# Kernel optimization log

Hardware: AMD Instinct MI355X
Metric: run time of the kernel (lower is better)

## Reference

```python
import jax, jax.numpy as jnp
import numpy as np

EPS_MASK = 1e-9   # module fills masked scores with eps, NOT -inf
LN_EPS = 1e-5

def _layer_norm(x, g, b):
    mu = jnp.mean(x, axis=-1, keepdims=True)
    var = jnp.mean(jnp.square(x - mu), axis=-1, keepdims=True)
    return (x - mu) * jax.lax.rsqrt(var + LN_EPS) * g + b

def _mha(q_in, k_in, v_in, wq, bq, wk, bk, wv, bv, wo, bo, mask, nhead):
    B, Sq, D = q_in.shape
    dk = D // nhead
    def proj(x, w, b):
        y = x @ w + b                                   # [B,S,D]
        return y.reshape(B, -1, nhead, dk).transpose(0, 2, 1, 3)  # [B,h,S,dk]
    q, k, v = proj(q_in, wq, bq), proj(k_in, wk, bk), proj(v_in, wv, bv)
    scores = jnp.einsum('bhqd,bhkd->bhqk', q, k) / np.sqrt(dk).astype(q.dtype)
    if mask is not None:
        scores = jnp.where(mask[:, None, :, :] == 0, jnp.asarray(EPS_MASK, scores.dtype), scores)
    p = jax.nn.softmax(scores, axis=-1)                 # dropout = identity (eval)
    x = jnp.einsum('bhqk,bhkd->bhqd', p, v)
    x = x.transpose(0, 2, 1, 3).reshape(B, Sq, D)
    return x @ wo + bo

def _forward_post(tgt, memory, tgt_pos, memory_pos, tgt_mask, memory_mask, p):
    nhead = 8
    # self-attention (q=k=tgt+pos, v=tgt)
    q = tgt + tgt_pos
    sa = _mha(q, q, tgt, p['sa_wq'], p['sa_bq'], p['sa_wk'], p['sa_bk'],
              p['sa_wv'], p['sa_bv'], p['sa_wo'], p['sa_bo'], tgt_mask, nhead)
    tgt = _layer_norm(tgt + sa, p['ln1_g'], p['ln1_b'])
    # cross-attention (q=tgt+tgt_pos, k=memory+memory_pos, v=memory)
    mq = tgt + tgt_pos
    mk = memory + memory_pos
    ca = _mha(mq, mk, memory, p['ca_wq'], p['ca_bq'], p['ca_wk'], p['ca_bk'],
              p['ca_wv'], p['ca_bv'], p['ca_wo'], p['ca_bo'], memory_mask, nhead)
    tgt = _layer_norm(tgt + ca, p['ln2_g'], p['ln2_b'])
    # FFN
    h = jax.nn.relu(tgt @ p['mlp_w1'] + p['mlp_b1'])
    ff = h @ p['mlp_w2'] + p['mlp_b2']
    return _layer_norm(tgt + ff, p['ln3_g'], p['ln3_b'])

def setup_inputs() -> dict:
    key = jax.random.key(0)
    B, S, M, D, H = 4, 1024, 1024, 512, 2048
    ks = iter(jax.random.split(key, 40))
    d = {
        'tgt': jax.random.normal(next(ks), (B, S, D), jnp.float32),
        'memory': jax.random.normal(next(ks), (B, M, D), jnp.float32),
        'tgt_pos': jax.random.normal(next(ks), (B, S, D), jnp.float32),
        'memory_pos': jax.random.normal(next(ks), (B, M, D), jnp.float32),
        'tgt_mask': jax.random.randint(next(ks), (B, S, S), 0, 2, jnp.int32),
        'memory_mask': jax.random.randint(next(ks), (B, S, M), 0, 2, jnp.int32),
    }
    for pre in ('sa', 'ca'):
        for nm in ('q', 'k', 'v', 'o'):
            d[f'{pre}_w{nm}'] = jax.random.normal(next(ks), (D, D), jnp.float32) * 0.02
            d[f'{pre}_b{nm}'] = jnp.zeros((D,), jnp.float32)
    for i in (1, 2, 3):
        d[f'ln{i}_g'] = jnp.ones((D,), jnp.float32)
        d[f'ln{i}_b'] = jnp.zeros((D,), jnp.float32)
    d['mlp_w1'] = jax.random.normal(next(ks), (D, H), jnp.float32) * 0.02
    d['mlp_b1'] = jnp.zeros((H,), jnp.float32)
    d['mlp_w2'] = jax.random.normal(next(ks), (H, D), jnp.float32) * 0.02
    d['mlp_b2'] = jnp.zeros((D,), jnp.float32)
    return d

def reference(tgt, memory, tgt_pos, memory_pos, tgt_mask, memory_mask,
              sa_wq, sa_bq, sa_wk, sa_bk, sa_wv, sa_bv, sa_wo, sa_bo,
              ca_wq, ca_bq, ca_wk, ca_bk, ca_wv, ca_bv, ca_wo, ca_bo,
              ln1_g, ln1_b, ln2_g, ln2_b, ln3_g, ln3_b,
              mlp_w1, mlp_b1, mlp_w2, mlp_b2):
    p = dict(sa_wq=sa_wq, sa_bq=sa_bq, sa_wk=sa_wk, sa_bk=sa_bk, sa_wv=sa_wv,
             sa_bv=sa_bv, sa_wo=sa_wo, sa_bo=sa_bo, ca_wq=ca_wq, ca_bq=ca_bq,
             ca_wk=ca_wk, ca_bk=ca_bk, ca_wv=ca_wv, ca_bv=ca_bv, ca_wo=ca_wo,
             ca_bo=ca_bo, ln1_g=ln1_g, ln1_b=ln1_b, ln2_g=ln2_g, ln2_b=ln2_b,
             ln3_g=ln3_g, ln3_b=ln3_b, mlp_w1=mlp_w1, mlp_b1=mlp_b1,
             mlp_w2=mlp_w2, mlp_b2=mlp_b2)
    return _forward_post(tgt, memory, tgt_pos, memory_pos, tgt_mask, memory_mask, p)
```

## Files before the change

kernel.cpp:

```cpp
#include <hip/hip_runtime.h>
#include <stdint.h>

typedef unsigned int u32;
typedef unsigned long long u64;
typedef unsigned short u16;
typedef __attribute__((ext_vector_type(8))) __bf16 bf16x8;
typedef __attribute__((ext_vector_type(4))) float f32x4;

#define DEV __device__ __forceinline__

DEV u16 f2bf(float f) {
    u32 x = __builtin_bit_cast(u32, f);
    u32 r = (x + 0x7FFFu + ((x >> 16) & 1u)) >> 16;
    return (u16)r;
}

DEV float bf2f(u16 x) {
    u32 u = (u32)x << 16;
    return __builtin_bit_cast(float, u);
}

DEV void unp8(uint4 u, float* f) {
    f[0] = bf2f((u16)u.x); f[1] = bf2f((u16)(u.x >> 16));
    f[2] = bf2f((u16)u.y); f[3] = bf2f((u16)(u.y >> 16));
    f[4] = bf2f((u16)u.z); f[5] = bf2f((u16)(u.z >> 16));
    f[6] = bf2f((u16)u.w); f[7] = bf2f((u16)(u.w >> 16));
}

DEV bf16x8 ldg8(const u16* p) {
    return __builtin_bit_cast(bf16x8, *(const uint4*)p);
}

DEV u32 pk2(float a, float b) {
    return (u32)f2bf(a) | ((u32)f2bf(b) << 16);
}

DEV void g2l16(const u16* g, u16* l) {
    __builtin_amdgcn_global_load_lds(
        (const __attribute__((address_space(1))) u32*)g,
        (__attribute__((address_space(3))) u32*)l, 16, 0, 0);
}

DEV f32x4 mfma16(bf16x8 a, bf16x8 b, f32x4 c) {
    return __builtin_amdgcn_mfma_f32_16x16x32_bf16(a, b, c, 0, 0, 0);
}

struct ProArgs {
    const float* w[10];
    u16* wtbase;
    const float4 *tgt, *tpos, *mem, *mpos;
    ushort4 *qin, *tgtb, *memb, *mkb, *tposb;
    const int4 *m1, *m2;
    u32 *o1, *o2;
};
__global__ __launch_bounds__(256) void prologue_kernel(ProArgs a) {
    const int bx = blockIdx.x, t = threadIdx.x;
    if (bx < 10240) {
        int z = bx >> 10, bxx = bx & 1023;
        int Kd = (z == 9) ? 2048 : 512;
        int Nd = (z == 8) ? 2048 : 512;
        size_t off = (z < 8) ? (size_t)z * 262144
                             : (z == 8 ? (size_t)2097152 : (size_t)3145728);
        u16* out = a.wtbase + off;
        int nx = Nd / 32;
        int txile = bxx % nx, tyile = bxx / nx;
        if (tyile >= Kd / 32) return;
        const float* w = a.w[z];
        __shared__ float tl[32][33];
        int tx = t & 31, ty = t >> 5;
#pragma unroll
        for (int j = 0; j < 4; ++j)
            tl[ty + j * 8][tx] = w[(size_t)(tyile * 32 + ty + j * 8) * Nd + txile * 32 + tx];
        __syncthreads();
#pragma unroll
        for (int j = 0; j < 4; ++j)
            out[(size_t)(txile * 32 + ty + j * 8) * Kd + tyile * 32 + tx] = f2bf(tl[tx][ty + j * 8]);
    } else if (bx < 12288) {
        int i = (bx - 10240) * 256 + t;
        float4 tt = a.tgt[i], p = a.tpos[i], m = a.mem[i], mp = a.mpos[i];
        a.qin[i]  = make_ushort4(f2bf(tt.x + p.x), f2bf(tt.y + p.y), f2bf(tt.z + p.z), f2bf(tt.w + p.w));
        a.tgtb[i] = make_ushort4(f2bf(tt.x), f2bf(tt.y), f2bf(tt.z), f2bf(tt.w));
        a.memb[i] = make_ushort4(f2bf(m.x), f2bf(m.y), f2bf(m.z), f2bf(m.w));
        a.mkb[i]  = make_ushort4(f2bf(m.x + mp.x), f2bf(m.y + mp.y), f2bf(m.z + mp.z), f2bf(m.w + mp.w));
        a.tposb[i]= make_ushort4(f2bf(p.x), f2bf(p.y), f2bf(p.z), f2bf(p.w));
    } else {
        int i = (bx - 12288) * 256 + t;
        const int n8 = 524288;
        bool first = i < n8;
        int idx = first ? i : i - n8;
        const int4* src = first ? a.m1 : a.m2;
        int4 x = src[idx * 2], y = src[idx * 2 + 1];
        u32 by = (u32)(x.x != 0) | ((u32)(x.y != 0) << 1) | ((u32)(x.z != 0) << 2) |
                 ((u32)(x.w != 0) << 3) | ((u32)(y.x != 0) << 4) | ((u32)(y.y != 0) << 5) |
                 ((u32)(y.z != 0) << 6) | ((u32)(y.w != 0) << 7);
        u32 w = by | (__shfl_down(by, 1) << 8) | (__shfl_down(by, 2) << 16) |
                (__shfl_down(by, 3) << 24);
        if ((t & 3) == 0) (first ? a.o1 : a.o2)[idx >> 2] = w;
    }
}

struct GemmSet {
    const u16* A; const u16* W; const float* bias; void* out;
    float oscale; int epi; int k0; int klen;
};
struct GemmArgs5 { GemmSet s[5]; };

template <int BM, int BN>
__global__ __launch_bounds__(256) void gemm_kernel(GemmArgs5 args, int M, int N, int Kd) {
    constexpr int MF = BM / 32, NF = BN / 32;
    const GemmSet gs = args.s[blockIdx.z];
    const u16* __restrict__ A = gs.A;
    const u16* __restrict__ W = gs.W;
    const int t = threadIdx.x;
    const int lane = t & 63;
    const int g = lane >> 4, r16 = lane & 15;
    const int wave = t >> 6;
    const int wm = wave >> 1, wn = wave & 1;
    const int nwg = gridDim.x * gridDim.y;
    const int fid = blockIdx.y * gridDim.x + blockIdx.x;
    const int qq = nwg >> 3;
    const int lid = (fid & 7) * qq + (fid >> 3);
    const int m0 = (lid / gridDim.x) * BM, n0 = (lid % gridDim.x) * BN;

    __shared__ __align__(16) u16 As[BM * 64];
    __shared__ __align__(16) u16 Bs[BN * 64];

    f32x4 acc[MF][NF];
#pragma unroll
    for (int m = 0; m < MF; ++m)
#pragma unroll
        for (int n = 0; n < NF; ++n) acc[m][n] = f32x4{0.f, 0.f, 0.f, 0.f};

    const int kend = gs.k0 + gs.klen;
    for (int kk = gs.k0; kk < kend; kk += 64) {
        __syncthreads();
#pragma unroll
        for (int i = 0; i < BM / 32; ++i) {
            int cid = t + i * 256, row = cid >> 3, c = cid & 7;
            g2l16(A + (size_t)(m0 + row) * Kd + kk + ((c ^ (row & 7)) << 3), &As[cid << 3]);
        }
#pragma unroll
        for (int i = 0; i < BN / 32; ++i) {
            int cid = t + i * 256, row = cid >> 3, c = cid & 7;
            g2l16(W + (size_t)(n0 + row) * Kd + kk + ((c ^ (row & 7)) << 3), &Bs[cid << 3]);
        }
        __syncthreads();
#pragma unroll
        for (int ks = 0; ks < 2; ++ks) {
            bf16x8 af[MF], bfr[NF];
#pragma unroll
            for (int m = 0; m < MF; ++m) {
                int row = wm * (MF * 16) + m * 16 + r16;
                af[m] = *(const bf16x8*)&As[(row << 6) + (((ks * 4 + g) ^ (row & 7)) << 3)];
            }
#pragma unroll
            for (int n = 0; n < NF; ++n) {
                int row = wn * (NF * 16) + n * 16 + r16;
                bfr[n] = *(const bf16x8*)&Bs[(row << 6) + (((ks * 4 + g) ^ (row & 7)) << 3)];
            }
#pragma unroll
            for (int m = 0; m < MF; ++m)
#pragma unroll
                for (int n = 0; n < NF; ++n)
                    acc[m][n] = mfma16(af[m], bfr[n], acc[m][n]);
        }
    }
    const int epi = gs.epi;
#pragma unroll
    for (int m = 0; m < MF; ++m) {
        int row0 = m0 + wm * (MF * 16) + m * 16 + g * 4;
#pragma unroll
        for (int n = 0; n < NF; ++n) {
            int col = n0 + wn * (NF * 16) + n * 16 + r16;
            float bv = gs.bias ? gs.bias[col] : 0.f;
            float v[4];
#pragma unroll
            for (int r = 0; r < 4; ++r) v[r] = (acc[m][n][r] + bv) * gs.oscale;
            if (epi == 1) {
#pragma unroll
                for (int r = 0; r < 4; ++r) v[r] = fmaxf(v[r], 0.f);
            }
            if (epi == 3) {
                int bb = row0 >> 10, s = row0 & 1023;
                u16* o = (u16*)gs.out +
                         ((size_t)(bb * 8 + (col >> 6)) * 64 + (col & 63)) * 1024 + s;
                *(ushort4*)o = make_ushort4(f2bf(v[0]), f2bf(v[1]), f2bf(v[2]), f2bf(v[3]));
            } else {
                u16* o = (u16*)gs.out;
#pragma unroll
                for (int r = 0; r < 4; ++r) o[(size_t)(row0 + r) * N + col] = f2bf(v[r]);
            }
        }
    }
}

__global__ __launch_bounds__(512, 4) void attn_part_kernel(
    const u16* __restrict__ Q, const u16* __restrict__ K,
    const u16* __restrict__ VT, const u32* __restrict__ mb,
    u16* __restrict__ OP, float2* __restrict__ ML) {
    constexpr int Lq = 1024, Lk = 1024, NCH = 8;
    const int t = threadIdx.x, lane = t & 63, wave = t >> 6;
    const int g = lane >> 4, r16 = lane & 15;
    const int h = blockIdx.x;
    const int b = blockIdx.y >> 1, p = blockIdx.y & 1;
    const int bh = b * 8 + h;
    const int q0 = blockIdx.z * 128 + wave * 16;
    const int kc0 = p * (Lk >> 1);

    __shared__ __align__(16) u16 Ks[2][64][64];
    __shared__ __align__(16) u16 Vs[2][64][64];
    __shared__ __align__(16) u16 Pl[8][16][72];

    const size_t qrow = (size_t)b * Lq + q0 + r16;
    const u16* qp = Q + qrow * 512 + h * 64 + g * 8;
    bf16x8 qb0 = ldg8(qp), qb1 = ldg8(qp + 32);
    const u32* mrow = mb + qrow * (Lk >> 5);

    const int sid = t & 255;
    const bool isK = t < 256;
    const int s1 = sid, s2 = sid + 256;
    const int r1 = s1 >> 3, c1 = s1 & 7;
    const int r2 = s2 >> 3, c2 = s2 & 7;
    const u16 *sgA, *sgB;
    if (isK) {
        const u16* kbase = K + (size_t)b * Lk * 512 + h * 64;
        sgA = kbase + (size_t)(kc0 + r1) * 512 + ((c1 ^ (r1 & 7)) << 3);
        sgB = kbase + (size_t)(kc0 + r2) * 512 + ((c2 ^ (r2 & 7)) << 3);
    } else {
        const u16* vbase = VT + (size_t)bh * 64 * Lk + kc0;
        sgA = vbase + (size_t)r1 * Lk + ((c1 ^ (r1 & 7)) << 3);
        sgB = vbase + (size_t)r2 * Lk + ((c2 ^ (r2 & 7)) << 3);
    }
    const size_t adv = isK ? (size_t)64 * 512 : 64;
    u16* const base = isK ? &Ks[0][0][0] : &Vs[0][0][0];
    u16* const slA = base + s1 * 8;
    u16* const slB = base + s2 * 8;

    f32x4 acc[4];
#pragma unroll
    for (int dt = 0; dt < 4; ++dt) acc[dt] = f32x4{0.f, 0.f, 0.f, 0.f};
    float mrun = -INFINITY, lrun = 0.f;
    const f32x4 zf = {0.f, 0.f, 0.f, 0.f};

    g2l16(sgA, slA);
    g2l16(sgB, slB);
    __syncthreads();

#pragma unroll
    for (int c = 0; c < NCH; ++c) {
        const int buf = c & 1, nbuf = buf ^ 1;
        const int kc = kc0 + c * 64;
        if (c + 1 < NCH) {
            g2l16(sgA + (size_t)(c + 1) * adv, slA + nbuf * 4096);
            g2l16(sgB + (size_t)(c + 1) * adv, slB + nbuf * 4096);
        }
        const u16* kb = &Ks[buf][0][0];
        const u16* vb = &Vs[buf][0][0];
        f32x4 s[4];
#pragma unroll
        for (int j = 0; j < 4; ++j) {
            int row = j * 16 + r16;
            bf16x8 ka0 = *(const bf16x8*)(kb + row * 64 + ((g ^ (row & 7)) << 3));
            bf16x8 ka1 = *(const bf16x8*)(kb + row * 64 + (((4 + g) ^ (row & 7)) << 3));
            s[j] = mfma16(ka0, qb0, zf);
            s[j] = mfma16(ka1, qb1, s[j]);
        }
        u32 mw0 = mrow[kc >> 5], mw1 = mrow[(kc >> 5) + 1];
        float sv[16];
#pragma unroll
        for (int j = 0; j < 4; ++j) {
            u32 w = (j < 2) ? mw0 : mw1;
            int bbase = (16 * j) & 31;
#pragma unroll
            for (int r = 0; r < 4; ++r) {
                int bit = bbase + g * 4 + r;
                sv[4 * j + r] = ((w >> bit) & 1) ? s[j][r] : 1e-9f;
            }
        }
        float tm = fmaxf(fmaxf(fmaxf(sv[0], sv[1]), fmaxf(sv[2], sv[3])),
                         fmaxf(fmaxf(sv[4], sv[5]), fmaxf(sv[6], sv[7])));
        float tm2 = fmaxf(fmaxf(fmaxf(sv[8], sv[9]), fmaxf(sv[10], sv[11])),
                          fmaxf(fmaxf(sv[12], sv[13]), fmaxf(sv[14], sv[15])));
        tm = fmaxf(tm, tm2);
        tm = fmaxf(tm, __shfl_xor(tm, 16));
        tm = fmaxf(tm, __shfl_xor(tm, 32));
        if (!__all(tm <= mrun + 8.f)) {
            float mn = fmaxf(mrun, tm);
            float alpha = __expf(mrun - mn);
            mrun = mn;
            lrun *= alpha;
#pragma unroll
            for (int r = 0; r < 4; ++r) {
                float ar = __shfl(alpha, g * 4 + r);
#pragma unroll
                for (int dt = 0; dt < 4; ++dt) acc[dt][r] *= ar;
            }
        }
        float ts = 0.f;
#pragma unroll
        for (int j = 0; j < 16; ++j) { sv[j] = __expf(sv[j] - mrun); ts += sv[j]; }
        ts += __shfl_xor(ts, 16);
        ts += __shfl_xor(ts, 32);
        lrun += ts;

#pragma unroll
        for (int j = 0; j < 4; ++j) {
            uint2 u;
            u.x = pk2(sv[4 * j], sv[4 * j + 1]);
            u.y = pk2(sv[4 * j + 2], sv[4 * j + 3]);
            *(uint2*)&Pl[wave][r16][16 * j + g * 4] = u;
        }
        bf16x8 pf0 = *(const bf16x8*)&Pl[wave][r16][g * 8];
        bf16x8 pf1 = *(const bf16x8*)&Pl[wave][r16][32 + g * 8];
#pragma unroll
        for (int dt = 0; dt < 4; ++dt) {
            int row = dt * 16 + r16;
            bf16x8 vf0 = *(const bf16x8*)(vb + row * 64 + ((g ^ (row & 7)) << 3));
            bf16x8 vf1 = *(const bf16x8*)(vb + row * 64 + (((4 + g) ^ (row & 7)) << 3));
            acc[dt] = mfma16(pf0, vf0, acc[dt]);
            acc[dt] = mfma16(pf1, vf1, acc[dt]);
        }
        __syncthreads();
    }

    if (lane < 16)
        ML[(size_t)p * 32768 + (size_t)bh * 1024 + q0 + lane] = make_float2(mrun, lrun);
    const size_t obase = (size_t)p * 2097152 + ((size_t)bh * 1024 + q0) * 64;
#pragma unroll
    for (int dt = 0; dt < 4; ++dt)
#pragma unroll
        for (int r = 0; r < 4; ++r)
            OP[obase + (size_t)(g * 4 + r) * 64 + dt * 16 + r16] = f2bf(acc[dt][r]);
}

__global__ __launch_bounds__(256) void attn_combine_kernel(
    const u16* __restrict__ OP, const float2* __restrict__ ML, u16* __restrict__ O) {
    int gid = blockIdx.x * 256 + threadIdx.x;
    int row = gid >> 3, seg = gid & 7;
    size_t idx = (size_t)row * 64 + seg * 8;
    float2 ml0 = ML[row], ml1 = ML[32768 + row];
    float M = fmaxf(ml0.x, ml1.x);
    float w0 = __expf(ml0.x - M), w1 = __expf(ml1.x - M);
    float rden = 1.f / (ml0.y * w0 + ml1.y * w1);
    w0 *= rden; w1 *= rden;
    float a[8], b[8];
    unp8(*(const uint4*)(OP + idx), a);
    unp8(*(const uint4*)(OP + 2097152 + idx), b);
    int bh = row >> 10, q = row & 1023;
    int bb = bh >> 3, h = bh & 7;
    u16* o = O + ((size_t)(bb * 1024 + q)) * 512 + h * 64 + seg * 8;
    uint4 r;
    r.x = pk2(a[0] * w0 + b[0] * w1, a[1] * w0 + b[1] * w1);
    r.y = pk2(a[2] * w0 + b[2] * w1, a[3] * w0 + b[3] * w1);
    r.z = pk2(a[4] * w0 + b[4] * w1, a[5] * w0 + b[5] * w1);
    r.w = pk2(a[6] * w0 + b[6] * w1, a[7] * w0 + b[7] * w1);
    *(uint4*)o = r;
}

template <int MODE>
__global__ __launch_bounds__(256) void ln_kernel(
    const u16* __restrict__ a, const u16* __restrict__ b1, const u16* __restrict__ b2,
    const float* __restrict__ gam, const float* __restrict__ bet,
    const u16* __restrict__ pos,
    u16* __restrict__ yb, u16* __restrict__ qb, float* __restrict__ yf) {
    const int lane = threadIdx.x & 63;
    const int row = blockIdx.x * 4 + (threadIdx.x >> 6);
    const size_t base = (size_t)row * 512 + lane * 8;
    float av[8], bv[8], cv[8];
    unp8(*(const uint4*)(a + base), av);
    unp8(*(const uint4*)(b1 + base), bv);
    unp8(*(const uint4*)(b2 + base), cv);
    float x[8];
#pragma unroll
    for (int j = 0; j < 8; ++j) x[j] = av[j] + bv[j] + cv[j];
    float s1 = 0.f, s2 = 0.f;
#pragma unroll
    for (int j = 0; j < 8; ++j) { s1 += x[j]; s2 += x[j] * x[j]; }
#pragma unroll
    for (int d = 1; d < 64; d <<= 1) { s1 += __shfl_xor(s1, d); s2 += __shfl_xor(s2, d); }
    float mean = s1 * (1.f / 512.f);
    float var = s2 * (1.f / 512.f) - mean * mean;
    float rs = rsqrtf(var + 1e-5f);
    float4 gv0 = ((const float4*)(gam + lane * 8))[0];
    float4 gv1 = ((const float4*)(gam + lane * 8))[1];
    float4 be0 = ((const float4*)(bet + lane * 8))[0];
    float4 be1 = ((const float4*)(bet + lane * 8))[1];
    float gg[8] = {gv0.x, gv0.y, gv0.z, gv0.w, gv1.x, gv1.y, gv1.z, gv1.w};
    float bb[8] = {be0.x, be0.y, be0.z, be0.w, be1.x, be1.y, be1.z, be1.w};
    float y[8];
#pragma unroll
    for (int j = 0; j < 8; ++j) y[j] = (x[j] - mean) * rs * gg[j] + bb[j];
    if (MODE == 2) {
        ((float4*)(yf + base))[0] = make_float4(y[0], y[1], y[2], y[3]);
        ((float4*)(yf + base))[1] = make_float4(y[4], y[5], y[6], y[7]);
        return;
    }
    uint4 r;
    r.x = pk2(y[0], y[1]); r.y = pk2(y[2], y[3]);
    r.z = pk2(y[4], y[5]); r.w = pk2(y[6], y[7]);
    *(uint4*)(yb + base) = r;
    if (MODE == 0) {
        float pv[8];
        unp8(*(const uint4*)(pos + base), pv);
        uint4 q;
        q.x = pk2(y[0] + pv[0], y[1] + pv[1]);
        q.y = pk2(y[2] + pv[2], y[3] + pv[3]);
        q.z = pk2(y[4] + pv[4], y[5] + pv[5]);
        q.w = pk2(y[6] + pv[6], y[7] + pv[7]);
        *(uint4*)(qb + base) = q;
    }
}

extern "C" void kernel_launch(void* const* d_in, const int* in_sizes, int n_in,
                              void* d_out, int out_size, void* d_ws, size_t ws_size,
                              hipStream_t stream) {
    (void)in_sizes; (void)n_in; (void)out_size; (void)ws_size;
    const float* tgt      = (const float*)d_in[0];
    const float* memory   = (const float*)d_in[1];
    const float* tgt_pos  = (const float*)d_in[2];
    const float* mem_pos  = (const float*)d_in[3];
    const int*   tgt_mask = (const int*)d_in[4];
    const int*   mem_mask = (const int*)d_in[5];
    const float* sa_b[4] = {(const float*)d_in[7], (const float*)d_in[9],
                            (const float*)d_in[11], (const float*)d_in[13]};
    const float* ca_b[4] = {(const float*)d_in[15], (const float*)d_in[17],
                            (const float*)d_in[19], (const float*)d_in[21]};
    const float* ln1_g = (const float*)d_in[22]; const float* ln1_b = (const float*)d_in[23];
    const float* ln2_g = (const float*)d_in[24]; const float* ln2_b = (const float*)d_in[25];
    const float* ln3_g = (const float*)d_in[26]; const float* ln3_b = (const float*)d_in[27];
    const float* mlp_b1 = (const float*)d_in[29];
    const float* mlp_b2 = (const float*)d_in[31];

    const size_t MiB = 1024 * 1024;
    char* ws = (char*)d_ws;
    u16*  WT  = (u16*)(ws + 0);
    u32*  MBS = (u32*)(ws + 8 * MiB);
    u32*  MBC = (u32*)(ws + 8 * MiB + 512 * 1024);
    u16*  QIN = (u16*)(ws + 9 * MiB);
    u16*  TGTB= (u16*)(ws + 13 * MiB);
    u16*  MEMB= (u16*)(ws + 17 * MiB);
    u16*  MKB = (u16*)(ws + 21 * MiB);
    u16*  QM  = (u16*)(ws + 25 * MiB);
    u16*  KMS = (u16*)(ws + 29 * MiB);
    u16*  KMC = (u16*)(ws + 33 * MiB);
    u16*  VTS = (u16*)(ws + 37 * MiB);
    u16*  VTC = (u16*)(ws + 41 * MiB);
    u16*  ATNB= (u16*)(ws + 45 * MiB);
    u16*  P1B = (u16*)(ws + 49 * MiB);
    u16*  X1B = (u16*)(ws + 53 * MiB);
    u16*  MQB = (u16*)(ws + 57 * MiB);
    u16*  X2B = (u16*)(ws + 61 * MiB);
    u16*  TPB = (u16*)(ws + 65 * MiB);
    u16*  P2B = (u16*)(ws + 69 * MiB);
    u16*  FFH = (u16*)(ws + 9 * MiB);
    u16*  OPB = (u16*)(ws + 96 * MiB);
    float2* MLB = (float2*)(ws + 120 * MiB);

    u16* wt[10];
    for (int z = 0; z < 8; ++z) wt[z] = WT + (size_t)z * 262144;
    wt[8] = WT + 2097152;
    wt[9] = WT + 3145728;

    ProArgs pa;
    pa.w[0] = (const float*)d_in[6];  pa.w[1] = (const float*)d_in[8];
    pa.w[2] = (const float*)d_in[10]; pa.w[3] = (const float*)d_in[12];
    pa.w[4] = (const float*)d_in[14]; pa.w[5] = (const float*)d_in[16];
    pa.w[6] = (const float*)d_in[18]; pa.w[7] = (const float*)d_in[20];
    pa.w[8] = (const float*)d_in[28]; pa.w[9] = (const float*)d_in[30];
    pa.wtbase = WT;
    pa.tgt = (const float4*)tgt; pa.tpos = (const float4*)tgt_pos;
    pa.mem = (const float4*)memory; pa.mpos = (const float4*)mem_pos;
    pa.qin = (ushort4*)QIN; pa.tgtb = (ushort4*)TGTB;
    pa.memb = (ushort4*)MEMB; pa.mkb = (ushort4*)MKB;
    pa.tposb = (ushort4*)TPB;
    pa.m1 = (const int4*)tgt_mask; pa.m2 = (const int4*)mem_mask;
    pa.o1 = MBS; pa.o2 = MBC;
    prologue_kernel<<<16384, 256, 0, stream>>>(pa);

    GemmArgs5 ga;
    ga.s[0] = {QIN,  wt[0], sa_b[0], QM,  0.125f, 0, 0, 512};
    ga.s[1] = {QIN,  wt[1], sa_b[1], KMS, 1.f,    0, 0, 512};
    ga.s[2] = {TGTB, wt[2], sa_b[2], VTS, 1.f,    3, 0, 512};
    ga.s[3] = {MKB,  wt[5], ca_b[1], KMC, 1.f,    0, 0, 512};
    ga.s[4] = {MEMB, wt[6], ca_b[2], VTC, 1.f,    3, 0, 512};
    gemm_kernel<128, 64><<<dim3(8, 32, 5), 256, 0, stream>>>(ga, 4096, 512, 512);
    attn_part_kernel<<<dim3(8, 8, 8), 512, 0, stream>>>(QM, KMS, VTS, MBS, OPB, MLB);
    attn_combine_kernel<<<1024, 256, 0, stream>>>(OPB, MLB, ATNB);
    ga.s[0] = {ATNB, wt[3], sa_b[3], P1B, 1.f, 0, 0,   256};
    ga.s[1] = {ATNB, wt[3], nullptr, P2B, 1.f, 0, 256, 256};
    ga.s[2] = ga.s[0]; ga.s[3] = ga.s[0]; ga.s[4] = ga.s[0];
    gemm_kernel<64, 64><<<dim3(8, 64, 2), 256, 0, stream>>>(ga, 4096, 512, 512);
    ln_kernel<0><<<1024, 256, 0, stream>>>(TGTB, P1B, P2B, ln1_g, ln1_b, TPB, X1B, MQB, nullptr);

    ga.s[0] = {MQB, wt[4], ca_b[0], QM, 0.125f, 0, 0, 512};
    ga.s[1] = ga.s[0]; ga.s[2] = ga.s[0]; ga.s[3] = ga.s[0]; ga.s[4] = ga.s[0];
    gemm_kernel<64, 64><<<dim3(8, 64, 1), 256, 0, stream>>>(ga, 4096, 512, 512);
    attn_part_kernel<<<dim3(8, 8, 8), 512, 0, stream>>>(QM, KMC, VTC, MBC, OPB, MLB);
    attn_combine_kernel<<<1024, 256, 0, stream>>>(OPB, MLB, ATNB);
    ga.s[0] = {ATNB, wt[7], ca_b[3], P1B, 1.f, 0, 0,   256};
    ga.s[1] = {ATNB, wt[7], nullptr, P2B, 1.f, 0, 256, 256};
    ga.s[2] = ga.s[0]; ga.s[3] = ga.s[0]; ga.s[4] = ga.s[0];
    gemm_kernel<64, 64><<<dim3(8, 64, 2), 256, 0, stream>>>(ga, 4096, 512, 512);
    ln_kernel<1><<<1024, 256, 0, stream>>>(X1B, P1B, P2B, ln2_g, ln2_b, nullptr, X2B, nullptr, nullptr);

    ga.s[0] = {X2B, wt[8], mlp_b1, FFH, 1.f, 1, 0, 512};
    ga.s[1] = ga.s[0]; ga.s[2] = ga.s[0]; ga.s[3] = ga.s[0]; ga.s[4] = ga.s[0];
    gemm_kernel<128, 64><<<dim3(32, 32, 1), 256, 0, stream>>>(ga, 4096, 2048, 512);
    ga.s[0] = {FFH, wt[9], mlp_b2, P1B, 1.f, 0, 0,    1024};
    ga.s[1] = {FFH, wt[9], nullptr, P2B, 1.f, 0, 1024, 1024};
    ga.s[2] = ga.s[0]; ga.s[3] = ga.s[0]; ga.s[4] = ga.s[0];
    gemm_kernel<64, 64><<<dim3(8, 64, 2), 256, 0, stream>>>(ga, 4096, 512, 2048);
    ln_kernel<2><<<1024, 256, 0, stream>>>(X2B, P1B, P2B, ln3_g, ln3_b, nullptr,
                                           nullptr, nullptr, (float*)d_out);
}
```

Before: 158.8 us.

## Split attention keys four ways and fold log2e into Q scale for exp2

The flash-attention partial kernel now splits the 1024 keys into four chunks instead of two, doubling the block count. The combine kernel merges four partial outputs using their running max and sum. Separately, the Q projection scale now includes log2(e), so the softmax uses the native exp2 instruction. The mask fill value and the rescale threshold are scaled to match. The extra split adds partial-output traffic and combine work, and relies on the OP/ML scratch buffers being large enough for four partitions.

```diff
diff --git a/kernel.cpp b/kernel.cpp
--- a/kernel.cpp
+++ b/kernel.cpp
@@ -33,6 +33,10 @@
 
 DEV u32 pk2(float a, float b) {
     return (u32)f2bf(a) | ((u32)f2bf(b) << 16);
+}
+
+DEV float ex2(float x) {
+    return __builtin_amdgcn_exp2f(x);
 }
 
 DEV void g2l16(const u16* g, u16* l) {
@@ -198,14 +202,16 @@
     const u16* __restrict__ Q, const u16* __restrict__ K,
     const u16* __restrict__ VT, const u32* __restrict__ mb,
     u16* __restrict__ OP, float2* __restrict__ ML) {
-    constexpr int Lq = 1024, Lk = 1024, NCH = 8;
+    constexpr int Lq = 1024, Lk = 1024, NCH = 4;
+    constexpr float MFILL = 1.442695041e-9f;
+    constexpr float DTHR  = 11.5415603f;
     const int t = threadIdx.x, lane = t & 63, wave = t >> 6;
     const int g = lane >> 4, r16 = lane & 15;
     const int h = blockIdx.x;
-    const int b = blockIdx.y >> 1, p = blockIdx.y & 1;
+    const int b = blockIdx.y >> 2, p = blockIdx.y & 3;
     const int bh = b * 8 + h;
     const int q0 = blockIdx.z * 128 + wave * 16;
-    const int kc0 = p * (Lk >> 1);
+    const int kc0 = p * (Lk >> 2);
 
     __shared__ __align__(16) u16 Ks[2][64][64];
     __shared__ __align__(16) u16 Vs[2][64][64];
@@ -274,7 +280,7 @@
 #pragma unroll
             for (int r = 0; r < 4; ++r) {
                 int bit = bbase + g * 4 + r;
-                sv[4 * j + r] = ((w >> bit) & 1) ? s[j][r] : 1e-9f;
+                sv[4 * j + r] = ((w >> bit) & 1) ? s[j][r] : MFILL;
             }
         }
         float tm = fmaxf(fmaxf(fmaxf(sv[0], sv[1]), fmaxf(sv[2], sv[3])),
@@ -284,9 +290,9 @@
         tm = fmaxf(tm, tm2);
         tm = fmaxf(tm, __shfl_xor(tm, 16));
         tm = fmaxf(tm, __shfl_xor(tm, 32));
-        if (!__all(tm <= mrun + 8.f)) {
+        if (!__all(tm <= mrun + DTHR)) {
             float mn = fmaxf(mrun, tm);
-            float alpha = __expf(mrun - mn);
+            float alpha = ex2(mrun - mn);
             mrun = mn;
             lrun *= alpha;
 #pragma unroll
@@ -298,7 +304,7 @@
         }
         float ts = 0.f;
 #pragma unroll
-        for (int j = 0; j < 16; ++j) { sv[j] = __expf(sv[j] - mrun); ts += sv[j]; }
+        for (int j = 0; j < 16; ++j) { sv[j] = ex2(sv[j] - mrun); ts += sv[j]; }
         ts += __shfl_xor(ts, 16);
         ts += __shfl_xor(ts, 32);
         lrun += ts;
@@ -338,22 +344,30 @@
     int gid = blockIdx.x * 256 + threadIdx.x;
     int row = gid >> 3, seg = gid & 7;
     size_t idx = (size_t)row * 64 + seg * 8;
-    float2 ml0 = ML[row], ml1 = ML[32768 + row];
-    float M = fmaxf(ml0.x, ml1.x);
-    float w0 = __expf(ml0.x - M), w1 = __expf(ml1.x - M);
-    float rden = 1.f / (ml0.y * w0 + ml1.y * w1);
-    w0 *= rden; w1 *= rden;
-    float a[8], b[8];
+    float2 ml0 = ML[row],          ml1 = ML[32768 + row];
+    float2 ml2 = ML[65536 + row],  ml3 = ML[98304 + row];
+    float M = fmaxf(fmaxf(ml0.x, ml1.x), fmaxf(ml2.x, ml3.x));
+    float w0 = ex2(ml0.x - M), w1 = ex2(ml1.x - M);
+    float w2 = ex2(ml2.x - M), w3 = ex2(ml3.x - M);
+    float rden = 1.f / (ml0.y * w0 + ml1.y * w1 + ml2.y * w2 + ml3.y * w3);
+    w0 *= rden; w1 *= rden; w2 *= rden; w3 *= rden;
+    float a[8], b[8], c[8], d[8];
     unp8(*(const uint4*)(OP + idx), a);
     unp8(*(const uint4*)(OP + 2097152 + idx), b);
+    unp8(*(const uint4*)(OP + 4194304 + idx), c);
+    unp8(*(const uint4*)(OP + 6291456 + idx), d);
     int bh = row >> 10, q = row & 1023;
     int bb = bh >> 3, h = bh & 7;
     u16* o = O + ((size_t)(bb * 1024 + q)) * 512 + h * 64 + seg * 8;
     uint4 r;
-    r.x = pk2(a[0] * w0 + b[0] * w1, a[1] * w0 + b[1] * w1);
-    r.y = pk2(a[2] * w0 + b[2] * w1, a[3] * w0 + b[3] * w1);
-    r.z = pk2(a[4] * w0 + b[4] * w1, a[5] * w0 + b[5] * w1);
-    r.w = pk2(a[6] * w0 + b[6] * w1, a[7] * w0 + b[7] * w1);
+    r.x = pk2(a[0] * w0 + b[0] * w1 + c[0] * w2 + d[0] * w3,
+              a[1] * w0 + b[1] * w1 + c[1] * w2 + d[1] * w3);
+    r.y = pk2(a[2] * w0 + b[2] * w1 + c[2] * w2 + d[2] * w3,
+              a[3] * w0 + b[3] * w1 + c[3] * w2 + d[3] * w3);
+    r.z = pk2(a[4] * w0 + b[4] * w1 + c[4] * w2 + d[4] * w3,
+              a[5] * w0 + b[5] * w1 + c[5] * w2 + d[5] * w3);
+    r.w = pk2(a[6] * w0 + b[6] * w1 + c[6] * w2 + d[6] * w3,
+              a[7] * w0 + b[7] * w1 + c[7] * w2 + d[7] * w3);
     *(uint4*)o = r;
 }
 
@@ -477,14 +491,15 @@
     pa.o1 = MBS; pa.o2 = MBC;
     prologue_kernel<<<16384, 256, 0, stream>>>(pa);
 
+    const float QSC = 0.125f * 1.44269504f;
     GemmArgs5 ga;
-    ga.s[0] = {QIN,  wt[0], sa_b[0], QM,  0.125f, 0, 0, 512};
-    ga.s[1] = {QIN,  wt[1], sa_b[1], KMS, 1.f,    0, 0, 512};
-    ga.s[2] = {TGTB, wt[2], sa_b[2], VTS, 1.f,    3, 0, 512};
-    ga.s[3] = {MKB,  wt[5], ca_b[1], KMC, 1.f,    0, 0, 512};
-    ga.s[4] = {MEMB, wt[6], ca_b[2], VTC, 1.f,    3, 0, 512};
+    ga.s[0] = {QIN,  wt[0], sa_b[0], QM,  QSC, 0, 0, 512};
+    ga.s[1] = {QIN,  wt[1], sa_b[1], KMS, 1.f, 0, 0, 512};
+    ga.s[2] = {TGTB, wt[2], sa_b[2], VTS, 1.f, 3, 0, 512};
+    ga.s[3] = {MKB,  wt[5], ca_b[1], KMC, 1.f, 0, 0, 512};
+    ga.s[4] = {MEMB, wt[6], ca_b[2], VTC, 1.f, 3, 0, 512};
     gemm_kernel<128, 64><<<dim3(8, 32, 5), 256, 0, stream>>>(ga, 4096, 512, 512);
-    attn_part_kernel<<<dim3(8, 8, 8), 512, 0, stream>>>(QM, KMS, VTS, MBS, OPB, MLB);
+    attn_part_kernel<<<dim3(8, 16, 8), 512, 0, stream>>>(QM, KMS, VTS, MBS, OPB, MLB);
     attn_combine_kernel<<<1024, 256, 0, stream>>>(OPB, MLB, ATNB);
     ga.s[0] = {ATNB, wt[3], sa_b[3], P1B, 1.f, 0, 0,   256};
     ga.s[1] = {ATNB, wt[3], nullptr, P2B, 1.f, 0, 256, 256};
@@ -492,10 +507,10 @@
     gemm_kernel<64, 64><<<dim3(8, 64, 2), 256, 0, stream>>>(ga, 4096, 512, 512);
     ln_kernel<0><<<1024, 256, 0, stream>>>(TGTB, P1B, P2B, ln1_g, ln1_b, TPB, X1B, MQB, nullptr);
 
-    ga.s[0] = {MQB, wt[4], ca_b[0], QM, 0.125f, 0, 0, 512};
+    ga.s[0] = {MQB, wt[4], ca_b[0], QM, QSC, 0, 0, 512};
     ga.s[1] = ga.s[0]; ga.s[2] = ga.s[0]; ga.s[3] = ga.s[0]; ga.s[4] = ga.s[0];
     gemm_kernel<64, 64><<<dim3(8, 64, 1), 256, 0, stream>>>(ga, 4096, 512, 512);
-    attn_part_kernel<<<dim3(8, 8, 8), 512, 0, stream>>>(QM, KMC, VTC, MBC, OPB, MLB);
+    attn_part_kernel<<<dim3(8, 16, 8), 512, 0, stream>>>(QM, KMC, VTC, MBC, OPB, MLB);
     attn_combine_kernel<<<1024, 256, 0, stream>>>(OPB, MLB, ATNB);
     ga.s[0] = {ATNB, wt[7], ca_b[3], P1B, 1.f, 0, 0,   256};
     ga.s[1] = {ATNB, wt[7], nullptr, P2B, 1.f, 0, 256, 256};
```

Result: slower. 163.8 us (+3.2%).
